# Kernel optimization log

Measured on AMD Instinct MI355X. Metric: run time of the kernel, lower is better.

## Reference

```python
import jax, jax.numpy as jnp
import numpy as np

K_NEIGHBORS = 5
WEIGHT = 0.5
EPS = 1e-12


def _l2_normalize(x):
    return x / jnp.maximum(jnp.linalg.norm(x, axis=1, keepdims=True), EPS)


def setup_inputs() -> dict:
    key = jax.random.key(0)
    k1, k2, k3, k4 = jax.random.split(key, 4)
    return {
        "hidden_current": jax.random.normal(k1, (4096, 768), dtype=jnp.float32),
        "hidden_previous": jax.random.normal(k2, (8192, 768), dtype=jnp.float32),
        "labels_current": jax.random.randint(k3, (4096,), 0, 100, dtype=jnp.int64),
        "labels_previous": jax.random.randint(k4, (8192,), 0, 100, dtype=jnp.int64),
    }


def reference(hidden_current, hidden_previous, labels_current, labels_previous):
    B_curr = hidden_current.shape[0]
    B_prev = hidden_previous.shape[0]

    # --- affinity from previous representations (no_grad in original) ---
    hp = _l2_normalize(jax.lax.stop_gradient(hidden_previous))
    dist_prev = 1.0 - hp @ hp.T                      # [B_prev, B_prev] cosine distance
    # smallest k+1 distances == largest k+1 of negated distances
    _, nbr = jax.lax.top_k(-dist_prev, K_NEIGHBORS + 1)
    nbr = nbr[:, 1:]                                 # drop self, [B_prev, K]
    same = labels_previous[:, None] == labels_previous[nbr]   # [B_prev, K]
    e = jnp.where(same, 1.0, -1.0).astype(jnp.float32)        # w - b
    rows = jnp.arange(B_prev)[:, None]
    affinity = jnp.zeros((B_prev, B_prev), dtype=jnp.float32).at[rows, nbr].set(e)

    # --- squared pairwise distances of normalized current representations ---
    hc = _l2_normalize(hidden_current)
    sq = jnp.sum(hc * hc, axis=1)
    d2 = jnp.maximum(sq[:, None] + sq[None, :] - 2.0 * (hc @ hc.T), 0.0)  # [B_curr, B_curr]

    loss = jnp.sum(affinity[:B_curr, :B_curr] * d2) / (B_curr * B_curr)
    return WEIGHT * loss
```

## Files before the change

### kernel.cpp

```cpp
#include <hip/hip_runtime.h>

#define BC 4096
#define BP 8192
#define D  768
#define KNB 5
#define TOPK 6
#define NT (BP / 128)

typedef __bf16 bf16x8 __attribute__((ext_vector_type(8)));
typedef float  f32x4  __attribute__((ext_vector_type(4)));

__device__ __forceinline__ unsigned short f2bf(float f) {
    unsigned int u = __float_as_uint(f);
    u += 0x7fffu + ((u >> 16) & 1u);
    return (unsigned short)(u >> 16);
}

__device__ __forceinline__ void gload16(const void* g, void* l) {
    __builtin_amdgcn_global_load_lds(
        (const __attribute__((address_space(1))) unsigned int*)g,
        (__attribute__((address_space(3))) unsigned int*)l, 16, 0, 0);
}

__device__ __forceinline__ void topk_insert(float v, int j, float* bv, int* bj) {
    #pragma unroll
    for (int q = TOPK - 1; q >= 1; q--) {
        bool up   = v > bv[q - 1];
        bool here = (v > bv[q]) && !up;
        bv[q] = up ? bv[q - 1] : (here ? v : bv[q]);
        bj[q] = up ? bj[q - 1] : (here ? j : bj[q]);
    }
    if (v > bv[0]) { bv[0] = v; bj[0] = j; }
}

__device__ __forceinline__ void topk_insert_u(unsigned v, unsigned* bk) {
    unsigned c = v;
    #pragma unroll
    for (int q = 0; q < TOPK; q++) {
        unsigned hi = (c > bk[q]) ? c : bk[q];
        c           = (c > bk[q]) ? bk[q] : c;
        bk[q] = hi;
    }
}

__global__ __launch_bounds__(256) void k_norm(const float* __restrict__ hp,
                                              const float* __restrict__ hc,
                                              unsigned short* __restrict__ hpnb,
                                              float* __restrict__ hcn,
                                              float* __restrict__ sqout,
                                              float* __restrict__ out) {
    int b = blockIdx.x;
    int t = threadIdx.x;
    if (b == 0 && t == 0) out[0] = 0.0f;
    bool isP = (b < BP);
    int row = isP ? b : (b - BP);
    const float* xr = (isP ? hp : hc) + (size_t)row * D;
    float v0 = xr[t], v1 = xr[t + 256], v2 = xr[t + 512];
    float s = v0 * v0 + v1 * v1 + v2 * v2;
    #pragma unroll
    for (int off = 32; off; off >>= 1) s += __shfl_xor(s, off, 64);
    __shared__ float wsum[4];
    if ((t & 63) == 0) wsum[t >> 6] = s;
    __syncthreads();
    float tot = wsum[0] + wsum[1] + wsum[2] + wsum[3];
    float rinv = 1.0f / fmaxf(sqrtf(tot), 1e-12f);
    if (isP) {
        unsigned short* yr = hpnb + (size_t)row * D;
        int rx = (row & 7) << 3;
        yr[t ^ rx]         = f2bf(v0 * rinv);
        yr[(t + 256) ^ rx] = f2bf(v1 * rinv);
        yr[(t + 512) ^ rx] = f2bf(v2 * rinv);
    } else {
        float* yr = hcn + (size_t)row * D;
        yr[t] = v0 * rinv; yr[t + 256] = v1 * rinv; yr[t + 512] = v2 * rinv;
        if (t == 0) sqout[row] = tot * rinv * rinv;
    }
}

__global__ __launch_bounds__(256, 4) void k_simtop(const unsigned short* __restrict__ hp,
                                                   float* __restrict__ candv,
                                                   int* __restrict__ candi) {
    __shared__ char smem[36864];
    unsigned short* sA = (unsigned short*)smem;
    unsigned short* sB = sA + 128 * 64;
    unsigned* sK = (unsigned*)smem;
    unsigned* mk = (unsigned*)(smem + 33280);

    const int t = threadIdx.x;
    const int l = t & 63;
    const int w = t >> 6;
    const int l15 = l & 15, quad = l >> 4;
    const int wr = w >> 1, wc = w & 1;

    int ri, ci;
    {
        int b = blockIdx.x;
        int super_id = (((b >> 9) & 3) << 3) | (b & 7);
        int within = (b >> 3) & 63;
        ri = (super_id >> 3) * 8 + (within >> 3);
        ci = (super_id & 7) * 8 + (within & 7);
    }

    const int srow = l >> 3, sch = l & 7;
    const unsigned short* Ag = hp + (size_t)(ri * 128 + w * 32 + srow) * D + sch * 8;
    const unsigned short* Bg = hp + (size_t)(ci * 128 + w * 32 + srow) * D + sch * 8;
    unsigned short* la = sA + (w * 32) * 64;
    unsigned short* lb = sB + (w * 32) * 64;

    f32x4 acc[4][4];
    #pragma unroll
    for (int i = 0; i < 4; i++)
        #pragma unroll
        for (int j = 0; j < 4; j++) acc[i][j] = (f32x4){4.f, 4.f, 4.f, 4.f};

    const int x7  = l15 & 7;
    const int ch0 = (quad ^ x7) * 16;
    const int ch1 = ((quad + 4) ^ x7) * 16;

    for (int kk = 0; kk < D; kk += 64) {
        __syncthreads();
        #pragma unroll
        for (int p = 0; p < 4; p++) {
            gload16(Ag + (size_t)(p * 8) * D + kk, la + (p * 8) * 64);
            gload16(Bg + (size_t)(p * 8) * D + kk, lb + (p * 8) * 64);
        }
        __syncthreads();
        #pragma unroll
        for (int ks = 0; ks < 2; ks++) {
            const int ch = ks ? ch1 : ch0;
            bf16x8 af[4], bfr[4];
            #pragma unroll
            for (int mi = 0; mi < 4; mi++)
                af[mi] = *(const bf16x8*)((const char*)sA + (wr * 64 + mi * 16 + l15) * 128 + ch);
            #pragma unroll
            for (int ni = 0; ni < 4; ni++)
                bfr[ni] = *(const bf16x8*)((const char*)sB + (wc * 64 + ni * 16 + l15) * 128 + ch);
            __builtin_amdgcn_s_setprio(1);
            #pragma unroll
            for (int mi = 0; mi < 4; mi++)
                #pragma unroll
                for (int ni = 0; ni < 4; ni++)
                    acc[mi][ni] = __builtin_amdgcn_mfma_f32_16x16x32_bf16(af[mi], bfr[ni], acc[mi][ni], 0, 0, 0);
            __builtin_amdgcn_s_setprio(0);
        }
    }

    unsigned bk[TOPK];
    #pragma unroll
    for (int s = 0; s < TOPK; s++) bk[s] = 0u;

    const int erow = t & 127, scb = (t >> 7) * 32;
    #pragma unroll
    for (int h = 0; h < 2; h++) {
        __syncthreads();
        if (wc == h) {
            #pragma unroll
            for (int ni = 0; ni < 4; ni++) {
                unsigned pk = (unsigned)(127 - h * 64 - ni * 16 - l15);
                #pragma unroll
                for (int mi = 0; mi < 4; mi++) {
                    int colb = ni * 16 + l15;
                    int rowb = wr * 64 + mi * 16 + quad * 4;
                    f32x4 v = acc[mi][ni];
                    #pragma unroll
                    for (int r = 0; r < 4; r++)
                        sK[(rowb + r) * 65 + colb] =
                            (__float_as_uint(v[r]) & 0xFFFFFF80u) | pk;
                }
            }
        }
        __syncthreads();
        const unsigned* rowp = sK + erow * 65 + scb;
        #pragma unroll
        for (int c = 0; c < 32; c++) topk_insert_u(rowp[c], bk);
    }

    __syncthreads();
    if (t >= 128) {
        #pragma unroll
        for (int s = 0; s < TOPK; s++) mk[(t - 128) * 7 + s] = bk[s];
    }
    __syncthreads();
    if (t < 128) {
        #pragma unroll
        for (int s0 = 0; s0 < TOPK; s0++) topk_insert_u(mk[t * 7 + s0], bk);
        size_t o = ((size_t)(ri * 128 + t) * NT + ci) * TOPK;
        #pragma unroll
        for (int s = 0; s < TOPK; s++) {
            unsigned k = bk[s];
            candv[o + s] = __uint_as_float(k & 0xFFFFFF80u);
            candi[o + s] = ci * 128 + 127 - (int)(k & 127u);
        }
    }
}

__global__ __launch_bounds__(256) void k_mergeloss(const float* __restrict__ candv,
                                                   const int* __restrict__ candi,
                                                   const float* __restrict__ hcn,
                                                   const float* __restrict__ sq,
                                                   const int* __restrict__ labp,
                                                   float* __restrict__ out) {
    __shared__ float bsum[4];
    const int w = threadIdx.x >> 6, lane = threadIdx.x & 63;
    const int i = blockIdx.x * 4 + w;

    const float* cv = candv + ((size_t)i * NT + lane) * TOPK;
    const int*   cj = candi + ((size_t)i * NT + lane) * TOPK;
    float bv[TOPK]; int bj[TOPK];
    #pragma unroll
    for (int s = 0; s < TOPK; s++) { bv[s] = cv[s]; bj[s] = cj[s]; }

    #pragma unroll
    for (int off = 1; off < 64; off <<= 1) {
        float pv[TOPK]; int pj[TOPK];
        #pragma unroll
        for (int s = 0; s < TOPK; s++) {
            pv[s] = __shfl_xor(bv[s], off, 64);
            pj[s] = __shfl_xor(bj[s], off, 64);
        }
        bool ilow = (lane & off) == 0;
        float av[TOPK], iv[TOPK]; int aj[TOPK], ij[TOPK];
        #pragma unroll
        for (int s = 0; s < TOPK; s++) {
            av[s] = ilow ? bv[s] : pv[s];  aj[s] = ilow ? bj[s] : pj[s];
            iv[s] = ilow ? pv[s] : bv[s];  ij[s] = ilow ? pj[s] : bj[s];
        }
        #pragma unroll
        for (int s = 0; s < TOPK; s++)
            if (iv[s] > av[TOPK - 1]) topk_insert(iv[s], ij[s], av, aj);
        #pragma unroll
        for (int s = 0; s < TOPK; s++) { bv[s] = av[s]; bj[s] = aj[s]; }
    }

    const float* hi = hcn + (size_t)i * D;
    float4 h0 = *(const float4*)(hi + lane * 4);
    float4 h1 = *(const float4*)(hi + lane * 4 + 256);
    float4 h2 = *(const float4*)(hi + lane * 4 + 512);
    float sqi = sq[i];
    int li = labp[i];
    float part = 0.f;
    float base = 0.f;
    #pragma unroll
    for (int s = 1; s <= KNB; s++) {
        int j = bj[s];
        if (j >= BC) continue;
        const float* hj = hcn + (size_t)j * D;
        float4 g0 = *(const float4*)(hj + lane * 4);
        float4 g1 = *(const float4*)(hj + lane * 4 + 256);
        float4 g2 = *(const float4*)(hj + lane * 4 + 512);
        float d = h0.x * g0.x + h0.y * g0.y + h0.z * g0.z + h0.w * g0.w
                + h1.x * g1.x + h1.y * g1.y + h1.z * g1.z + h1.w * g1.w
                + h2.x * g2.x + h2.y * g2.y + h2.z * g2.z + h2.w * g2.w;
        float e = (li == labp[j]) ? 1.0f : -1.0f;
        part += e * (-2.0f) * d;
        if (lane == 0) base += e * (sqi + sq[j]);
    }
    part += base;
    #pragma unroll
    for (int off = 32; off; off >>= 1) part += __shfl_xor(part, off, 64);
    if (lane == 0) bsum[w] = part;
    __syncthreads();
    if (threadIdx.x == 0) {
        float s = bsum[0] + bsum[1] + bsum[2] + bsum[3];
        unsafeAtomicAdd(out, 0.5f * s / ((float)BC * (float)BC));
    }
}

extern "C" void kernel_launch(void* const* d_in, const int* in_sizes, int n_in,
                              void* d_out, int out_size, void* d_ws, size_t ws_size,
                              hipStream_t stream) {
    const float* hc   = (const float*)d_in[0];
    const float* hp   = (const float*)d_in[1];
    const int*   labp = (const int*)d_in[3];
    float* out = (float*)d_out;

    unsigned short* hpnb = (unsigned short*)d_ws;
    float* hcn  = (float*)(hpnb + (size_t)BP * D);
    float* sq   = hcn + (size_t)BC * D;
    float* candv = sq + BC;
    int*   candi = (int*)(candv + (size_t)BC * NT * TOPK);

    k_norm<<<dim3(BP + BC), dim3(256), 0, stream>>>(hp, hc, hpnb, hcn, sq, out);
    k_simtop<<<dim3(2048), dim3(256), 0, stream>>>(hpnb, candv, candi);
    k_mergeloss<<<dim3(BC / 4), dim3(256), 0, stream>>>(candv, candi, hcn, sq, labp, out);
}
```

Measured before the change: 163.3 us.

## Enlarge similarity GEMM tile to 256x256 with double-buffered async LDS pipeline

The similarity/top-k kernel now computes 256x256 output tiles per 512-thread block instead of 128x128 per 256-thread block. K-slices are double-buffered in 128KB of LDS, and global loads are interleaved with MFMA phases using explicit waitcnt and barriers. This is meant to raise operand reuse and hide load latency. In exchange it uses much more LDS and registers, runs only 512 blocks, and has a more complex synchronization schedule that could be fragile.

After: 165.6 us. No clear change (+1.4%).

```diff
diff --git a/kernel.cpp b/kernel.cpp
--- a/kernel.cpp
+++ b/kernel.cpp
@@ -6,6 +6,8 @@
 #define KNB 5
 #define TOPK 6
 #define NT (BP / 128)
+#define NKT (D / 64)
+#define NIT (NKT / 2)
 
 typedef __bf16 bf16x8 __attribute__((ext_vector_type(8)));
 typedef float  f32x4  __attribute__((ext_vector_type(4)));
@@ -77,119 +79,178 @@
     }
 }
 
-__global__ __launch_bounds__(256, 4) void k_simtop(const unsigned short* __restrict__ hp,
+__global__ __launch_bounds__(512, 2) void k_simtop(const unsigned short* __restrict__ hp,
                                                    float* __restrict__ candv,
                                                    int* __restrict__ candi) {
-    __shared__ char smem[36864];
-    unsigned short* sA = (unsigned short*)smem;
-    unsigned short* sB = sA + 128 * 64;
-    unsigned* sK = (unsigned*)smem;
-    unsigned* mk = (unsigned*)(smem + 33280);
+    __shared__ char smem[139264];
 
     const int t = threadIdx.x;
     const int l = t & 63;
-    const int w = t >> 6;
+    const int wid = t >> 6;
     const int l15 = l & 15, quad = l >> 4;
-    const int wr = w >> 1, wc = w & 1;
-
-    int ri, ci;
+    const int wr = wid >> 2, wc = wid & 3;
+
+    int ri2, ci2;
     {
         int b = blockIdx.x;
-        int super_id = (((b >> 9) & 3) << 3) | (b & 7);
-        int within = (b >> 3) & 63;
-        ri = (super_id >> 3) * 8 + (within >> 3);
-        ci = (super_id & 7) * 8 + (within & 7);
-    }
-
-    const int srow = l >> 3, sch = l & 7;
-    const unsigned short* Ag = hp + (size_t)(ri * 128 + w * 32 + srow) * D + sch * 8;
-    const unsigned short* Bg = hp + (size_t)(ci * 128 + w * 32 + srow) * D + sch * 8;
-    unsigned short* la = sA + (w * 32) * 64;
-    unsigned short* lb = sB + (w * 32) * 64;
-
-    f32x4 acc[4][4];
-    #pragma unroll
-    for (int i = 0; i < 4; i++)
-        #pragma unroll
-        for (int j = 0; j < 4; j++) acc[i][j] = (f32x4){4.f, 4.f, 4.f, 4.f};
+        int super_id = (((b >> 7) & 3) << 3) | (b & 7);
+        int within = (b >> 3) & 15;
+        ri2 = (super_id >> 3) * 4 + (within >> 2);
+        ci2 = (super_id & 7) * 4 + (within & 3);
+    }
+
+    const unsigned short* As = hp + (size_t)(ri2 * 256 + (t >> 3)) * D + (t & 7) * 8;
+    const unsigned short* Bs = hp + (size_t)(ci2 * 256 + (t >> 3)) * D + (t & 7) * 8;
+    char* ldsbase = smem + wid * 1024;
+
+#define STAGE(buf, kt, c) do {                                                        \
+    const unsigned short* _s = ((c) < 2 ? As : Bs) + (size_t)(((c) & 1) * 128) * D + (kt) * 64; \
+    char* _d = ldsbase + (buf) * 65536 + ((c) >= 2 ? 32768 : 0) + ((c) & 1) * 16384;  \
+    gload16(_s, _d);                                                                  \
+    gload16(_s + 64 * D, _d + 8192);                                                  \
+} while (0)
 
     const int x7  = l15 & 7;
     const int ch0 = (quad ^ x7) * 16;
     const int ch1 = ((quad + 4) ^ x7) * 16;
-
-    for (int kk = 0; kk < D; kk += 64) {
+    const int aRow = (wr * 128 + l15) << 7;
+    const int bRow = 32768 + ((wc * 64 + l15) << 7);
+
+#define READ_AH(dst, h, bb)                                               \
+    _Pragma("unroll")                                                     \
+    for (int mi = 0; mi < 4; mi++) {                                      \
+        const char* _p = smem + (bb) + aRow + (((h) * 64 + mi * 16) << 7);\
+        dst[mi][0] = *(const bf16x8*)(_p + ch0);                          \
+        dst[mi][1] = *(const bf16x8*)(_p + ch1);                          \
+    }
+
+#define READ_BH(dst, h, bb)                                               \
+    _Pragma("unroll")                                                     \
+    for (int ni = 0; ni < 2; ni++) {                                      \
+        const char* _p = smem + (bb) + bRow + (((h) * 32 + ni * 16) << 7);\
+        dst[ni][0] = *(const bf16x8*)(_p + ch0);                          \
+        dst[ni][1] = *(const bf16x8*)(_p + ch1);                          \
+    }
+
+#define MFMA_Q(afr, bfr, mh, nh)                                                      \
+    _Pragma("unroll")                                                                 \
+    for (int mi = 0; mi < 4; mi++)                                                    \
+    _Pragma("unroll")                                                                 \
+    for (int ni = 0; ni < 2; ni++)                                                    \
+    _Pragma("unroll")                                                                 \
+    for (int ks = 0; ks < 2; ks++)                                                    \
+        acc[(mh) * 4 + mi][(nh) * 2 + ni] = __builtin_amdgcn_mfma_f32_16x16x32_bf16(  \
+            afr[mi][ks], bfr[ni][ks], acc[(mh) * 4 + mi][(nh) * 2 + ni], 0, 0, 0);
+
+#define PH_TOP()  do { __builtin_amdgcn_s_barrier();                                  \
+                       asm volatile("s_waitcnt lgkmcnt(0)" ::: "memory");             \
+                       __builtin_amdgcn_sched_barrier(0);                             \
+                       __builtin_amdgcn_s_setprio(1); } while (0)
+#define PH_END()  do { __builtin_amdgcn_s_setprio(0);                                 \
+                       __builtin_amdgcn_sched_barrier(0); } while (0)
+
+    f32x4 acc[8][4];
+    #pragma unroll
+    for (int i = 0; i < 8; i++)
+        #pragma unroll
+        for (int j = 0; j < 4; j++) acc[i][j] = (f32x4){4.f, 4.f, 4.f, 4.f};
+
+    STAGE(0, 0, 0); STAGE(0, 0, 1); STAGE(0, 0, 2); STAGE(0, 0, 3);
+    STAGE(1, 1, 0); STAGE(1, 1, 1); STAGE(1, 1, 2); STAGE(1, 1, 3);
+    asm volatile("s_waitcnt vmcnt(8)" ::: "memory");
+    __builtin_amdgcn_s_barrier();
+
+    bf16x8 a0[4][2], a1[4][2], b0v[2][2], b1v[2][2];
+
+    for (int it = 0; it < NIT; ++it) {
+        const int kt0 = 2 * it;
+        const bool pf = (it < NIT - 1);
+        READ_AH(a0, 0, 0); READ_BH(b0v, 0, 0);
+        PH_TOP(); MFMA_Q(a0, b0v, 0, 0); PH_END();
+        __builtin_amdgcn_s_barrier();
+        READ_BH(b1v, 1, 0);
+        PH_TOP(); MFMA_Q(a0, b1v, 0, 1); PH_END();
+        __builtin_amdgcn_s_barrier();
+        READ_AH(a1, 1, 0);
+        if (pf) STAGE(0, kt0 + 2, 2);
+        PH_TOP(); MFMA_Q(a1, b1v, 1, 1); PH_END();
+        __builtin_amdgcn_s_barrier();
+        if (pf) STAGE(0, kt0 + 2, 3);
+        PH_TOP(); MFMA_Q(a1, b0v, 1, 0); PH_END();
+        if (pf) { asm volatile("s_waitcnt vmcnt(4)" ::: "memory"); }
+        else    { asm volatile("s_waitcnt vmcnt(0)" ::: "memory"); }
+        __builtin_amdgcn_s_barrier();
+        READ_AH(a0, 0, 65536); READ_BH(b0v, 0, 65536);
+        if (pf) STAGE(0, kt0 + 2, 0);
+        PH_TOP(); MFMA_Q(a0, b0v, 0, 0); PH_END();
+        __builtin_amdgcn_s_barrier();
+        READ_BH(b1v, 1, 65536);
+        if (pf) STAGE(0, kt0 + 2, 1);
+        PH_TOP(); MFMA_Q(a0, b1v, 0, 1); PH_END();
+        __builtin_amdgcn_s_barrier();
+        READ_AH(a1, 1, 65536);
+        if (pf) { STAGE(1, kt0 + 3, 2); STAGE(1, kt0 + 3, 3); }
+        PH_TOP(); MFMA_Q(a1, b1v, 1, 1); PH_END();
+        __builtin_amdgcn_s_barrier();
+        if (pf) { STAGE(1, kt0 + 3, 0); STAGE(1, kt0 + 3, 1); }
+        PH_TOP(); MFMA_Q(a1, b0v, 1, 0); PH_END();
+        asm volatile("s_waitcnt vmcnt(8)" ::: "memory");
+        __builtin_amdgcn_s_barrier();
+    }
+
+#undef STAGE
+#undef READ_AH
+#undef READ_BH
+#undef MFMA_Q
+#undef PH_TOP
+#undef PH_END
+
+    unsigned* sS = (unsigned*)smem;
+    unsigned* mk = (unsigned*)(smem + 132096);
+    const int myH = wc >> 1;
+    const int colbase = (wc & 1) * 64;
+
+    #pragma unroll
+    for (int H = 0; H < 2; H++) {
         __syncthreads();
-        #pragma unroll
-        for (int p = 0; p < 4; p++) {
-            gload16(Ag + (size_t)(p * 8) * D + kk, la + (p * 8) * 64);
-            gload16(Bg + (size_t)(p * 8) * D + kk, lb + (p * 8) * 64);
-        }
-        __syncthreads();
-        #pragma unroll
-        for (int ks = 0; ks < 2; ks++) {
-            const int ch = ks ? ch1 : ch0;
-            bf16x8 af[4], bfr[4];
-            #pragma unroll
-            for (int mi = 0; mi < 4; mi++)
-                af[mi] = *(const bf16x8*)((const char*)sA + (wr * 64 + mi * 16 + l15) * 128 + ch);
-            #pragma unroll
-            for (int ni = 0; ni < 4; ni++)
-                bfr[ni] = *(const bf16x8*)((const char*)sB + (wc * 64 + ni * 16 + l15) * 128 + ch);
-            __builtin_amdgcn_s_setprio(1);
-            #pragma unroll
-            for (int mi = 0; mi < 4; mi++)
-                #pragma unroll
-                for (int ni = 0; ni < 4; ni++)
-                    acc[mi][ni] = __builtin_amdgcn_mfma_f32_16x16x32_bf16(af[mi], bfr[ni], acc[mi][ni], 0, 0, 0);
-            __builtin_amdgcn_s_setprio(0);
-        }
-    }
-
-    unsigned bk[TOPK];
-    #pragma unroll
-    for (int s = 0; s < TOPK; s++) bk[s] = 0u;
-
-    const int erow = t & 127, scb = (t >> 7) * 32;
-    #pragma unroll
-    for (int h = 0; h < 2; h++) {
-        __syncthreads();
-        if (wc == h) {
+        if (myH == H) {
             #pragma unroll
             for (int ni = 0; ni < 4; ni++) {
-                unsigned pk = (unsigned)(127 - h * 64 - ni * 16 - l15);
+                int colL = colbase + ni * 16 + l15;
+                unsigned pk = (unsigned)(127 - colL);
                 #pragma unroll
-                for (int mi = 0; mi < 4; mi++) {
-                    int colb = ni * 16 + l15;
-                    int rowb = wr * 64 + mi * 16 + quad * 4;
+                for (int mi = 0; mi < 8; mi++) {
+                    int rowb = wr * 128 + mi * 16 + quad * 4;
                     f32x4 v = acc[mi][ni];
                     #pragma unroll
                     for (int r = 0; r < 4; r++)
-                        sK[(rowb + r) * 65 + colb] =
+                        sS[(rowb + r) * 129 + colL] =
                             (__float_as_uint(v[r]) & 0xFFFFFF80u) | pk;
                 }
             }
         }
         __syncthreads();
-        const unsigned* rowp = sK + erow * 65 + scb;
-        #pragma unroll
-        for (int c = 0; c < 32; c++) topk_insert_u(rowp[c], bk);
-    }
-
-    __syncthreads();
-    if (t >= 128) {
-        #pragma unroll
-        for (int s = 0; s < TOPK; s++) mk[(t - 128) * 7 + s] = bk[s];
-    }
-    __syncthreads();
-    if (t < 128) {
-        #pragma unroll
-        for (int s0 = 0; s0 < TOPK; s0++) topk_insert_u(mk[t * 7 + s0], bk);
-        size_t o = ((size_t)(ri * 128 + t) * NT + ci) * TOPK;
-        #pragma unroll
-        for (int s = 0; s < TOPK; s++) {
-            unsigned k = bk[s];
-            candv[o + s] = __uint_as_float(k & 0xFFFFFF80u);
-            candi[o + s] = ci * 128 + 127 - (int)(k & 127u);
+        unsigned bk[TOPK];
+        #pragma unroll
+        for (int s = 0; s < TOPK; s++) bk[s] = 0u;
+        const unsigned* rowp = sS + (t & 255) * 129 + (t >> 8) * 64;
+        #pragma unroll
+        for (int c = 0; c < 64; c++) topk_insert_u(rowp[c], bk);
+        if (t >= 256) {
+            #pragma unroll
+            for (int s = 0; s < TOPK; s++) mk[(t - 256) * 7 + s] = bk[s];
+        }
+        __syncthreads();
+        if (t < 256) {
+            #pragma unroll
+            for (int s0 = 0; s0 < TOPK; s0++) topk_insert_u(mk[t * 7 + s0], bk);
+            size_t o = ((size_t)(ri2 * 256 + t) * NT + (ci2 * 2 + H)) * TOPK;
+            #pragma unroll
+            for (int s = 0; s < TOPK; s++) {
+                unsigned k = bk[s];
+                candv[o + s] = __uint_as_float(k & 0xFFFFFF80u);
+                candi[o + s] = ci2 * 256 + H * 128 + 127 - (int)(k & 127u);
+            }
         }
     }
 }
@@ -281,6 +342,6 @@
     int*   candi = (int*)(candv + (size_t)BC * NT * TOPK);
 
     k_norm<<<dim3(BP + BC), dim3(256), 0, stream>>>(hp, hc, hpnb, hcn, sq, out);
-    k_simtop<<<dim3(2048), dim3(256), 0, stream>>>(hpnb, candv, candi);
+    k_simtop<<<dim3(512), dim3(512), 0, stream>>>(hpnb, candv, candi);
     k_mergeloss<<<dim3(BC / 4), dim3(256), 0, stream>>>(candv, candi, hcn, sq, labp, out);
 }
```

## Exploit Gram matrix symmetry to skip mirrored similarity tiles

Applied to the files above, without the earlier changes.

The similarity top-k kernel now launches blocks only over upper-triangular tile pairs (ri<=ci) instead of the full 32x64 grid, using a triangular index decode. For off-diagonal tiles whose column tile falls in the current-batch range, it also scans the tile column-wise to produce top-k candidates for the mirrored rows. This cuts the matmul work by reusing each tile for both orientations. The cost is extra column scans and syncs, a serial while-loop index decode, and the loss of the previous swizzled block ordering for cache locality.

Measured after the change: 172.6 us. 1.06x slower.

```diff
diff --git a/kernel.cpp b/kernel.cpp
--- a/kernel.cpp
+++ b/kernel.cpp
@@ -6,6 +6,7 @@
 #define KNB 5
 #define TOPK 6
 #define NT (BP / 128)
+#define NBLK 1552
 
 typedef __bf16 bf16x8 __attribute__((ext_vector_type(8)));
 typedef float  f32x4  __attribute__((ext_vector_type(4)));
@@ -94,12 +95,13 @@
 
     int ri, ci;
     {
-        int b = blockIdx.x;
-        int super_id = (((b >> 9) & 3) << 3) | (b & 7);
-        int within = (b >> 3) & 63;
-        ri = (super_id >> 3) * 8 + (within >> 3);
-        ci = (super_id & 7) * 8 + (within & 7);
-    }
+        int n = blockIdx.x;
+        int m = (n & 7) * 194 + (n >> 3);
+        int r = 0, base = 0;
+        while (m - base >= 64 - r) { base += 64 - r; r++; }
+        ri = r; ci = r + (m - base);
+    }
+    const bool twoScan = (ci > ri) && (ci < 32);
 
     const int srow = l >> 3, sch = l & 7;
     const unsigned short* Ag = hp + (size_t)(ri * 128 + w * 32 + srow) * D + sch * 8;
@@ -173,6 +175,37 @@
         const unsigned* rowp = sK + erow * 65 + scb;
         #pragma unroll
         for (int c = 0; c < 32; c++) topk_insert_u(rowp[c], bk);
+
+        if (twoScan) {
+            unsigned ck[TOPK];
+            #pragma unroll
+            for (int s = 0; s < TOPK; s++) ck[s] = 0u;
+            if (t < 128) {
+                const int col = t & 63, rh = (t >> 6) & 1;
+                const unsigned* colp = sK + (rh * 64) * 65 + col;
+                const unsigned pk0 = (unsigned)(127 - rh * 64);
+                #pragma unroll
+                for (int r = 0; r < 64; r++)
+                    topk_insert_u((colp[r * 65] & 0xFFFFFF80u) | (pk0 - r), ck);
+            }
+            __syncthreads();
+            if (t >= 64 && t < 128) {
+                #pragma unroll
+                for (int s = 0; s < TOPK; s++) mk[(t - 64) * 7 + s] = ck[s];
+            }
+            __syncthreads();
+            if (t < 64) {
+                #pragma unroll
+                for (int s0 = 0; s0 < TOPK; s0++) topk_insert_u(mk[t * 7 + s0], ck);
+                size_t o = ((size_t)(ci * 128 + h * 64 + t) * NT + ri) * TOPK;
+                #pragma unroll
+                for (int s = 0; s < TOPK; s++) {
+                    unsigned k = ck[s];
+                    candv[o + s] = __uint_as_float(k & 0xFFFFFF80u);
+                    candi[o + s] = ri * 128 + 127 - (int)(k & 127u);
+                }
+            }
+        }
     }
 
     __syncthreads();
@@ -281,6 +314,6 @@
     int*   candi = (int*)(candv + (size_t)BC * NT * TOPK);
 
     k_norm<<<dim3(BP + BC), dim3(256), 0, stream>>>(hp, hc, hpnb, hcn, sq, out);
-    k_simtop<<<dim3(2048), dim3(256), 0, stream>>>(hpnb, candv, candi);
+    k_simtop<<<dim3(NBLK), dim3(256), 0, stream>>>(hpnb, candv, candi);
     k_mergeloss<<<dim3(BC / 4), dim3(256), 0, stream>>>(candv, candi, hcn, sq, labp, out);
 }
```
